# Kernel tuning notes

Hardware: AMD Instinct MI355X
Metric: run time of the kernel (lower is better)

## Reference

```python
import jax, jax.numpy as jnp
import numpy as np

B, S, HID = 1, 4096, 2048
NH, NKV, D = 16, 4, 128           # num_heads, num_kv_heads, head_dim
QPG = NH // NKV                   # q heads per kv group
GROUP = (QPG + 2) * D             # fused per-group width: Q..Q K V
TOTAL = NKV * GROUP


def setup_inputs() -> dict:
    key = jax.random.key(0)
    k0, k1, k2 = jax.random.split(key, 3)
    x = jax.random.normal(k0, (B, S, HID), dtype=jnp.float32)
    weight_qkv = jax.random.normal(k1, (TOTAL, HID), dtype=jnp.float32) * 0.02
    weight_proj = jax.random.normal(k2, (HID, NH * D), dtype=jnp.float32) * 0.02
    return {"x": x, "weight_qkv": weight_qkv, "weight_proj": weight_proj}


def reference(x, weight_qkv, weight_proj):
    b, s, _ = x.shape
    # fused QKV projection, grouped layout: [b, s, NKV, (QPG+2)*D]
    qkv = jnp.einsum('bsh,ph->bsp', x, weight_qkv).reshape(b, s, NKV, GROUP)
    q = qkv[..., : QPG * D].reshape(b, s, NKV, QPG, D)      # [b,s,g,q,d]
    k = qkv[..., QPG * D:(QPG + 1) * D]                      # [b,s,g,d]
    v = qkv[..., (QPG + 1) * D:]                             # [b,s,g,d]

    scale = 1.0 / jnp.sqrt(jnp.float32(D))
    # GQA causal attention (ring attention at cp_size=1 == full causal attn)
    scores = jnp.einsum('bsgqd,btgd->bgqst', q, k) * scale   # [b,g,q,s,s]
    causal = jnp.tril(jnp.ones((s, s), dtype=bool))
    scores = jnp.where(causal, scores, jnp.finfo(scores.dtype).min)
    attn = jax.nn.softmax(scores, axis=-1)
    out = jnp.einsum('bgqst,btgd->bsgqd', attn, v)           # [b,s,g,q,d]
    out = out.reshape(b, s, NH * D)
    return jnp.einsum('bse,he->bsh', out, weight_proj)       # [b,s,HID]
```

## Files before the change

### kernel.cpp

```cpp
#include <hip/hip_runtime.h>
#include <hip/hip_bf16.h>
#include <stdint.h>

typedef __attribute__((ext_vector_type(8))) short short8;
typedef __attribute__((ext_vector_type(4))) float f32x4;

#define S_LEN   4096
#define HID_DIM 2048
#define NHEAD   16
#define NKV     4
#define DHEAD   128
#define QPG     4
#define GROUP   768
#define TOTAL   3072

__device__ __forceinline__ ushort f2bf(float f) {
    union { float f; uint32_t u; } c; c.f = f;
    uint32_t u = c.u;
    u += 0x7fff + ((u >> 16) & 1);
    return (ushort)(u >> 16);
}

__device__ __forceinline__ void gld_lds16(const void* g, void* l) {
    __builtin_amdgcn_global_load_lds(
        (const __attribute__((address_space(1))) void*)g,
        (__attribute__((address_space(3))) void*)l, 16, 0, 0);
}

__global__ __launch_bounds__(256)
void cvt_f32_bf16(const float* __restrict__ src, ushort* __restrict__ dst,
                  int n4, int mode)
{
    int i = blockIdx.x * blockDim.x + threadIdx.x;
    int stride = gridDim.x * blockDim.x;
    for (; i < n4; i += stride) {
        float sc = 1.0f;
        if (mode == 1) {
            int row = i >> 9;
            sc = ((row % GROUP) < QPG * DHEAD) ? 0.088388347648318447f : 1.0f;
        }
        float4 v = ((const float4*)src)[i];
        ushort4 o;
        o.x = f2bf(v.x * sc); o.y = f2bf(v.y * sc);
        o.z = f2bf(v.z * sc); o.w = f2bf(v.w * sc);
        ((ushort4*)dst)[i] = o;
    }
}

__global__ __launch_bounds__(256)
void zero_f4(float4* __restrict__ p, int n4)
{
    int i = blockIdx.x * blockDim.x + threadIdx.x;
    int stride = gridDim.x * blockDim.x;
    float4 z = {0.f, 0.f, 0.f, 0.f};
    for (; i < n4; i += stride) p[i] = z;
}

__device__ __forceinline__ void store_c(ushort* C, size_t idx, float v) { C[idx] = f2bf(v); }
__device__ __forceinline__ void store_c(float*  C, size_t idx, float v) { C[idx] = v; }

template <typename OutT, bool WRITE_VT>
__global__ __launch_bounds__(256, 2)
void gemm_bt(const ushort* __restrict__ A, const ushort* __restrict__ B,
             OutT* __restrict__ C, ushort* __restrict__ VT,
             int M, int N, int K)
{
    __shared__ alignas(16) ushort Asl[128 * 32];
    __shared__ alignas(16) ushort Bsl[128 * 32];

    const int tid  = threadIdx.x;
    const int wave = tid >> 6;
    const int lane = tid & 63;
    const int quad = lane >> 4;
    const int l15  = lane & 15;
    const int wr   = wave >> 1;
    const int wc   = wave & 1;
    const int m0   = blockIdx.y * 128;
    const int n0   = blockIdx.x * 128;

    f32x4 acc[4][4];
#pragma unroll
    for (int i = 0; i < 4; i++)
#pragma unroll
        for (int j = 0; j < 4; j++) acc[i][j] = (f32x4)0.0f;

    for (int kb = 0; kb < K; kb += 32) {
        __syncthreads();
#pragma unroll
        for (int r = 0; r < 2; r++) {
            int idx = tid + r * 256;
            int row = idx >> 2, c8 = idx & 3;
            char* la = (char*)Asl + (size_t)(wave * 64 + r * 256) * 16;
            char* lb = (char*)Bsl + (size_t)(wave * 64 + r * 256) * 16;
            gld_lds16(A + (size_t)(m0 + row) * K + kb + c8 * 8, la);
            gld_lds16(B + (size_t)(n0 + row) * K + kb + c8 * 8, lb);
        }
        __syncthreads();

        short8 af[4], bf[4];
#pragma unroll
        for (int i = 0; i < 4; i++)
            af[i] = *(const short8*)(&Asl[(wr * 64 + i * 16 + l15) * 32 + quad * 8]);
#pragma unroll
        for (int j = 0; j < 4; j++)
            bf[j] = *(const short8*)(&Bsl[(wc * 64 + j * 16 + l15) * 32 + quad * 8]);
#pragma unroll
        for (int i = 0; i < 4; i++)
#pragma unroll
            for (int j = 0; j < 4; j++)
                acc[i][j] = __builtin_amdgcn_mfma_f32_16x16x32_bf16(
                    af[i], bf[j], acc[i][j], 0, 0, 0);
    }

    const bool v_block = WRITE_VT && ((n0 >> 7) % 6 == 5);
    if (!v_block) {
#pragma unroll
        for (int i = 0; i < 4; i++)
#pragma unroll
            for (int j = 0; j < 4; j++)
#pragma unroll
                for (int r = 0; r < 4; r++) {
                    int row = m0 + wr * 64 + i * 16 + quad * 4 + r;
                    int col = n0 + wc * 64 + j * 16 + l15;
                    store_c(C, (size_t)row * N + col, acc[i][j][r]);
                }
    } else {
        int g = (n0 >> 7) / 6;
#pragma unroll
        for (int i = 0; i < 4; i++)
#pragma unroll
            for (int j = 0; j < 4; j++) {
                int d    = wc * 64 + j * 16 + l15;
                int row0 = m0 + wr * 64 + i * 16 + quad * 4;
                ushort4 pk;
                pk.x = f2bf(acc[i][j][0]); pk.y = f2bf(acc[i][j][1]);
                pk.z = f2bf(acc[i][j][2]); pk.w = f2bf(acc[i][j][3]);
                *(ushort4*)(VT + (size_t)(g * 128 + d) * S_LEN + row0) = pk;
            }
    }
}

__global__ __launch_bounds__(256, 2)
void flash_attn(const ushort* __restrict__ qkv, const ushort* __restrict__ VT,
                ushort* __restrict__ out, float* __restrict__ o_slot,
                float* __restrict__ l_slot)
{
    const int b    = blockIdx.x;
    const int head = b >> 5;
    const int pair = (b >> 1) & 15;
    const int half = b & 1;
    const int g    = head >> 2;
    const int qh   = head & 3;
    const int p_h  = 31 - pair;
    const int H    = 2 * p_h + 2;
    const int slot = head * 16 + pair;

    const int tid  = threadIdx.x;
    const int wave = tid >> 6;
    const int lane = tid & 63;
    const int quad = lane >> 4;
    const int l15  = lane & 15;

    __shared__ alignas(16) ushort Kl[64][136];
    __shared__ alignas(16) ushort Vt[128][72];
    __shared__ alignas(16) ushort Pl[4][32][66];

    int seg_p[2], seg_t0[2], seg_t1[2], seg_part[2];
    int nseg;
    if (half == 0) {
        nseg = 1;
        seg_p[0] = p_h;  seg_t0[0] = 0;  seg_t1[0] = 33;           seg_part[0] = 1;
    } else {
        nseg = 2;
        seg_p[0] = p_h;  seg_t0[0] = 33; seg_t1[0] = H;            seg_part[0] = 1;
        seg_p[1] = pair; seg_t0[1] = 0;  seg_t1[1] = 2 * pair + 2; seg_part[1] = 0;
    }

    const int koff = g * GROUP + QPG * DHEAD;

    for (int s = 0; s < nseg; s++) {
        const int p  = seg_p[s];
        const int t0 = seg_t0[s];
        const int t1 = seg_t1[s];
        const int q0 = p * 128;
        const int base = q0 + wave * 32;

        short8 qf[2][4];
#pragma unroll
        for (int nq = 0; nq < 2; nq++) {
            int row = base + nq * 16 + l15;
            const ushort* qp = qkv + (size_t)row * TOTAL + g * GROUP + qh * DHEAD + quad * 8;
#pragma unroll
            for (int ks = 0; ks < 4; ks++)
                qf[nq][ks] = *(const short8*)(qp + ks * 32);
        }

        f32x4 o[2][8];
#pragma unroll
        for (int oq = 0; oq < 2; oq++)
#pragma unroll
            for (int df = 0; df < 8; df++) o[oq][df] = (f32x4)0.0f;
        float l_vec[2] = {0.0f, 0.0f};

        float4 kpre[4], vpre[4];
#pragma unroll
        for (int r = 0; r < 4; r++) {
            int c = tid + r * 256;
            int kr = c >> 4, kc = c & 15;
            kpre[r] = *(const float4*)(qkv + (size_t)(t0 * 64 + kr) * TOTAL + koff + kc * 8);
            int vd = c >> 3, vc = c & 7;
            vpre[r] = *(const float4*)(VT + (size_t)(g * 128 + vd) * S_LEN + t0 * 64 + vc * 8);
        }

        for (int t = t0; t < t1; t++) {
            __syncthreads();
#pragma unroll
            for (int r = 0; r < 4; r++) {
                int c = tid + r * 256;
                int kr = c >> 4, kc = c & 15;
                *(float4*)(&Kl[kr][kc * 8]) = kpre[r];
                int vd = c >> 3, vc = c & 7;
                *(float4*)(&Vt[vd][vc * 8]) = vpre[r];
            }
            __syncthreads();

            if (t + 1 < t1) {
                const int j1 = (t + 1) * 64;
#pragma unroll
                for (int r = 0; r < 4; r++) {
                    int c = tid + r * 256;
                    int kr = c >> 4, kc = c & 15;
                    kpre[r] = *(const float4*)(qkv + (size_t)(j1 + kr) * TOTAL + koff + kc * 8);
                    int vd = c >> 3, vc = c & 7;
                    vpre[r] = *(const float4*)(VT + (size_t)(g * 128 + vd) * S_LEN + j1 + vc * 8);
                }
            }

            const int j0 = t * 64;
            f32x4 sacc[4][2];
#pragma unroll
            for (int mk = 0; mk < 4; mk++)
#pragma unroll
                for (int nq = 0; nq < 2; nq++) sacc[mk][nq] = (f32x4)0.0f;
#pragma unroll
            for (int mk = 0; mk < 4; mk++)
#pragma unroll
                for (int ks = 0; ks < 4; ks++) {
                    short8 kf = *(const short8*)(&Kl[mk * 16 + l15][ks * 32 + quad * 8]);
#pragma unroll
                    for (int nq = 0; nq < 2; nq++)
                        sacc[mk][nq] = __builtin_amdgcn_mfma_f32_16x16x32_bf16(
                            kf, qf[nq][ks], sacc[mk][nq], 0, 0, 0);
                }

#pragma unroll
            for (int nq = 0; nq < 2; nq++) {
                const int qg = base + nq * 16 + l15;
#pragma unroll
                for (int mk = 0; mk < 4; mk++) {
                    float e0, e1, e2, e3;
                    if (j0 + mk * 16 + 15 > base + nq * 16) {
                        int kv = j0 + mk * 16 + quad * 4;
                        e0 = (kv + 0 > qg) ? 0.0f : __expf(sacc[mk][nq][0]);
                        e1 = (kv + 1 > qg) ? 0.0f : __expf(sacc[mk][nq][1]);
                        e2 = (kv + 2 > qg) ? 0.0f : __expf(sacc[mk][nq][2]);
                        e3 = (kv + 3 > qg) ? 0.0f : __expf(sacc[mk][nq][3]);
                    } else {
                        e0 = __expf(sacc[mk][nq][0]);
                        e1 = __expf(sacc[mk][nq][1]);
                        e2 = __expf(sacc[mk][nq][2]);
                        e3 = __expf(sacc[mk][nq][3]);
                    }
                    l_vec[nq] += (e0 + e1) + (e2 + e3);
                    ushort4 pk;
                    pk.x = f2bf(e0); pk.y = f2bf(e1);
                    pk.z = f2bf(e2); pk.w = f2bf(e3);
                    *(ushort4*)(&Pl[wave][nq * 16 + l15][mk * 16 + quad * 4]) = pk;
                }
            }

#pragma unroll
            for (int ks = 0; ks < 2; ks++) {
                short8 pf[2];
#pragma unroll
                for (int oq = 0; oq < 2; oq++)
                    pf[oq] = *(const short8*)(&Pl[wave][oq * 16 + l15][ks * 32 + quad * 8]);
#pragma unroll
                for (int df = 0; df < 8; df++) {
                    short8 vf = *(const short8*)(&Vt[df * 16 + l15][ks * 32 + quad * 8]);
#pragma unroll
                    for (int oq = 0; oq < 2; oq++)
                        o[oq][df] = __builtin_amdgcn_mfma_f32_16x16x32_bf16(
                            pf[oq], vf, o[oq][df], 0, 0, 0);
                }
            }
        }

        float l_full[2];
#pragma unroll
        for (int nq = 0; nq < 2; nq++) {
            float l = l_vec[nq];
            l += __shfl_xor(l, 16);
            l += __shfl_xor(l, 32);
            l_full[nq] = l;
        }

        if (seg_part[s]) {
#pragma unroll
            for (int nq = 0; nq < 2; nq++)
                if (quad == 0)
                    atomicAdd(&l_slot[slot * 128 + wave * 32 + nq * 16 + l15], l_full[nq]);
#pragma unroll
            for (int oq = 0; oq < 2; oq++)
#pragma unroll
                for (int r = 0; r < 4; r++) {
                    int row_l = wave * 32 + oq * 16 + quad * 4 + r;
#pragma unroll
                    for (int df = 0; df < 8; df++)
                        atomicAdd(&o_slot[((size_t)slot * 128 + row_l) * 128
                                          + df * 16 + l15], o[oq][df][r]);
                }
        } else {
#pragma unroll
            for (int oq = 0; oq < 2; oq++)
#pragma unroll
                for (int r = 0; r < 4; r++) {
                    float lq = __shfl(l_full[oq], quad * 4 + r);
                    float inv = 1.0f / lq;
                    int row = base + oq * 16 + quad * 4 + r;
#pragma unroll
                    for (int df = 0; df < 8; df++) {
                        float v = o[oq][df][r] * inv;
                        out[(size_t)row * (NHEAD * DHEAD) + head * DHEAD
                            + df * 16 + l15] = f2bf(v);
                    }
                }
        }
    }
}

__global__ __launch_bounds__(256)
void fixup_norm(const float* __restrict__ o_slot, const float* __restrict__ l_slot,
                ushort* __restrict__ attn)
{
    const int slot = blockIdx.x;
    const int head = slot >> 4;
    const int pair = slot & 15;
    const int q0   = (31 - pair) * 128;
    const int t    = threadIdx.x;
#pragma unroll 4
    for (int i = 0; i < 64; i++) {
        int idx = i * 256 + t;
        int row = idx >> 7, d = idx & 127;
        float l = l_slot[slot * 128 + row];
        float v = o_slot[(size_t)slot * 16384 + idx] / l;
        attn[(size_t)(q0 + row) * HID_DIM + head * DHEAD + d] = f2bf(v);
    }
}

extern "C" void kernel_launch(void* const* d_in, const int* in_sizes, int n_in,
                              void* d_out, int out_size, void* d_ws, size_t ws_size,
                              hipStream_t stream)
{
    const float* x     = (const float*)d_in[0];
    const float* wqkv  = (const float*)d_in[1];
    const float* wproj = (const float*)d_in[2];
    float* outp = (float*)d_out;

    const size_t n_x     = (size_t)S_LEN * HID_DIM;
    const size_t n_wqkv  = (size_t)TOTAL * HID_DIM;
    const size_t n_wproj = (size_t)HID_DIM * HID_DIM;
    const size_t n_qkv   = (size_t)S_LEN * TOTAL;
    const size_t n_attn  = (size_t)S_LEN * HID_DIM;

    ushort* xb     = (ushort*)d_ws;
    ushort* wqkvb  = xb + n_x;
    ushort* qkv    = wqkvb + n_wqkv;
    ushort* attn   = qkv + n_qkv;
    ushort* vt     = attn + n_attn;
    float* o_slot  = (float*)xb;
    float* l_slot  = (float*)wqkvb;
    ushort* wprojb = wqkvb;

    cvt_f32_bf16<<<2048, 256, 0, stream>>>(x, xb, (int)(n_x / 4), 0);
    cvt_f32_bf16<<<2048, 256, 0, stream>>>(wqkv, wqkvb, (int)(n_wqkv / 4), 1);

    gemm_bt<ushort, true><<<dim3(TOTAL / 128, S_LEN / 128), 256, 0, stream>>>(
        xb, wqkvb, qkv, vt, S_LEN, TOTAL, HID_DIM);

    zero_f4<<<1024, 256, 0, stream>>>((float4*)o_slot, 256 * 16384 / 4);
    zero_f4<<<64, 256, 0, stream>>>((float4*)l_slot, 256 * 128 / 4);

    flash_attn<<<512, 256, 0, stream>>>(qkv, vt, attn, o_slot, l_slot);
    fixup_norm<<<256, 256, 0, stream>>>(o_slot, l_slot, attn);

    cvt_f32_bf16<<<2048, 256, 0, stream>>>(wproj, wprojb, (int)(n_wproj / 4), 0);
    gemm_bt<float, false><<<dim3(HID_DIM / 128, S_LEN / 128), 256, 0, stream>>>(
        attn, wprojb, outp, nullptr, S_LEN, HID_DIM, HID_DIM);
}
```

Baseline: 430.5 us.

## Use exp2 softmax, per-half partial outputs, and 192-wide QKV GEMM tiles

Result: no change. 425.3 us (-1.2%).

```diff
diff --git a/kernel.cpp b/kernel.cpp
--- a/kernel.cpp
+++ b/kernel.cpp
@@ -14,11 +14,17 @@
 #define GROUP   768
 #define TOTAL   3072
 
+#define EXP2F(x) __builtin_amdgcn_exp2f(x)
+
 __device__ __forceinline__ ushort f2bf(float f) {
     union { float f; uint32_t u; } c; c.f = f;
     uint32_t u = c.u;
     u += 0x7fff + ((u >> 16) & 1);
     return (ushort)(u >> 16);
+}
+__device__ __forceinline__ float bf2f(ushort u) {
+    union { uint32_t u; float f; } c; c.u = ((uint32_t)u) << 16;
+    return c.f;
 }
 
 __device__ __forceinline__ void gld_lds16(const void* g, void* l) {
@@ -37,7 +43,7 @@
         float sc = 1.0f;
         if (mode == 1) {
             int row = i >> 9;
-            sc = ((row % GROUP) < QPG * DHEAD) ? 0.088388347648318447f : 1.0f;
+            sc = ((row % GROUP) < QPG * DHEAD) ? 0.12751744157413583f : 1.0f;
         }
         float4 v = ((const float4*)src)[i];
         ushort4 o;
@@ -47,26 +53,17 @@
     }
 }
 
-__global__ __launch_bounds__(256)
-void zero_f4(float4* __restrict__ p, int n4)
-{
-    int i = blockIdx.x * blockDim.x + threadIdx.x;
-    int stride = gridDim.x * blockDim.x;
-    float4 z = {0.f, 0.f, 0.f, 0.f};
-    for (; i < n4; i += stride) p[i] = z;
-}
-
 __device__ __forceinline__ void store_c(ushort* C, size_t idx, float v) { C[idx] = f2bf(v); }
 __device__ __forceinline__ void store_c(float*  C, size_t idx, float v) { C[idx] = v; }
 
-template <typename OutT, bool WRITE_VT>
+template <typename OutT, int NJ, bool WRITE_VT>
 __global__ __launch_bounds__(256, 2)
 void gemm_bt(const ushort* __restrict__ A, const ushort* __restrict__ B,
              OutT* __restrict__ C, ushort* __restrict__ VT,
              int M, int N, int K)
 {
     __shared__ alignas(16) ushort Asl[128 * 32];
-    __shared__ alignas(16) ushort Bsl[128 * 32];
+    __shared__ alignas(16) ushort Bsl[NJ * 32 * 32];
 
     const int tid  = threadIdx.x;
     const int wave = tid >> 6;
@@ -76,74 +73,76 @@
     const int wr   = wave >> 1;
     const int wc   = wave & 1;
     const int m0   = blockIdx.y * 128;
-    const int n0   = blockIdx.x * 128;
-
-    f32x4 acc[4][4];
+    const int n0   = blockIdx.x * (32 * NJ);
+
+    f32x4 acc[4][NJ];
 #pragma unroll
     for (int i = 0; i < 4; i++)
 #pragma unroll
-        for (int j = 0; j < 4; j++) acc[i][j] = (f32x4)0.0f;
+        for (int j = 0; j < NJ; j++) acc[i][j] = (f32x4)0.0f;
 
     for (int kb = 0; kb < K; kb += 32) {
         __syncthreads();
 #pragma unroll
-        for (int r = 0; r < 2; r++) {
-            int idx = tid + r * 256;
-            int row = idx >> 2, c8 = idx & 3;
-            char* la = (char*)Asl + (size_t)(wave * 64 + r * 256) * 16;
-            char* lb = (char*)Bsl + (size_t)(wave * 64 + r * 256) * 16;
-            gld_lds16(A + (size_t)(m0 + row) * K + kb + c8 * 8, la);
-            gld_lds16(B + (size_t)(n0 + row) * K + kb + c8 * 8, lb);
+        for (int k = 0; k < 2 + NJ / 2; k++) {
+            int idx = k * 256 + tid;
+            if (idx < 512) {
+                const ushort* g = A + (size_t)(m0 + (idx >> 2)) * K + kb + (idx & 3) * 8;
+                gld_lds16(g, (char*)Asl + (size_t)(k * 256 + wave * 64) * 16);
+            } else {
+                int j = idx - 512;
+                const ushort* g = B + (size_t)(n0 + (j >> 2)) * K + kb + (j & 3) * 8;
+                gld_lds16(g, (char*)Bsl + (size_t)((k - 2) * 256 + wave * 64) * 16);
+            }
         }
         __syncthreads();
 
-        short8 af[4], bf[4];
+        short8 af[4], bf[NJ];
 #pragma unroll
         for (int i = 0; i < 4; i++)
             af[i] = *(const short8*)(&Asl[(wr * 64 + i * 16 + l15) * 32 + quad * 8]);
 #pragma unroll
-        for (int j = 0; j < 4; j++)
-            bf[j] = *(const short8*)(&Bsl[(wc * 64 + j * 16 + l15) * 32 + quad * 8]);
+        for (int j = 0; j < NJ; j++)
+            bf[j] = *(const short8*)(&Bsl[(wc * 16 * NJ + j * 16 + l15) * 32 + quad * 8]);
 #pragma unroll
         for (int i = 0; i < 4; i++)
 #pragma unroll
-            for (int j = 0; j < 4; j++)
+            for (int j = 0; j < NJ; j++)
                 acc[i][j] = __builtin_amdgcn_mfma_f32_16x16x32_bf16(
                     af[i], bf[j], acc[i][j], 0, 0, 0);
     }
 
-    const bool v_block = WRITE_VT && ((n0 >> 7) % 6 == 5);
-    if (!v_block) {
-#pragma unroll
-        for (int i = 0; i < 4; i++)
-#pragma unroll
-            for (int j = 0; j < 4; j++)
-#pragma unroll
-                for (int r = 0; r < 4; r++) {
-                    int row = m0 + wr * 64 + i * 16 + quad * 4 + r;
-                    int col = n0 + wc * 64 + j * 16 + l15;
-                    store_c(C, (size_t)row * N + col, acc[i][j][r]);
-                }
-    } else {
-        int g = (n0 >> 7) / 6;
-#pragma unroll
-        for (int i = 0; i < 4; i++)
-#pragma unroll
-            for (int j = 0; j < 4; j++) {
-                int d    = wc * 64 + j * 16 + l15;
+#pragma unroll
+    for (int j = 0; j < NJ; j++) {
+        const int colb = n0 + wc * 16 * NJ + j * 16;
+        const int cgrp = colb % GROUP;
+        if (WRITE_VT && cgrp >= (QPG + 1) * DHEAD) {
+            const int g = colb / GROUP;
+            const int d = cgrp - (QPG + 1) * DHEAD + l15;
+#pragma unroll
+            for (int i = 0; i < 4; i++) {
                 int row0 = m0 + wr * 64 + i * 16 + quad * 4;
                 ushort4 pk;
                 pk.x = f2bf(acc[i][j][0]); pk.y = f2bf(acc[i][j][1]);
                 pk.z = f2bf(acc[i][j][2]); pk.w = f2bf(acc[i][j][3]);
                 *(ushort4*)(VT + (size_t)(g * 128 + d) * S_LEN + row0) = pk;
             }
+        } else {
+#pragma unroll
+            for (int i = 0; i < 4; i++)
+#pragma unroll
+                for (int r = 0; r < 4; r++) {
+                    int row = m0 + wr * 64 + i * 16 + quad * 4 + r;
+                    store_c(C, (size_t)row * N + colb + l15, acc[i][j][r]);
+                }
+        }
     }
 }
 
 __global__ __launch_bounds__(256, 2)
 void flash_attn(const ushort* __restrict__ qkv, const ushort* __restrict__ VT,
-                ushort* __restrict__ out, float* __restrict__ o_slot,
-                float* __restrict__ l_slot)
+                ushort* __restrict__ out, ushort* __restrict__ o_part,
+                float* __restrict__ l_part)
 {
     const int b    = blockIdx.x;
     const int head = b >> 5;
@@ -153,7 +152,7 @@
     const int qh   = head & 3;
     const int p_h  = 31 - pair;
     const int H    = 2 * p_h + 2;
-    const int slot = head * 16 + pair;
+    const int hslot = (head * 16 + pair) * 2 + half;
 
     const int tid  = threadIdx.x;
     const int wave = tid >> 6;
@@ -261,15 +260,15 @@
                     float e0, e1, e2, e3;
                     if (j0 + mk * 16 + 15 > base + nq * 16) {
                         int kv = j0 + mk * 16 + quad * 4;
-                        e0 = (kv + 0 > qg) ? 0.0f : __expf(sacc[mk][nq][0]);
-                        e1 = (kv + 1 > qg) ? 0.0f : __expf(sacc[mk][nq][1]);
-                        e2 = (kv + 2 > qg) ? 0.0f : __expf(sacc[mk][nq][2]);
-                        e3 = (kv + 3 > qg) ? 0.0f : __expf(sacc[mk][nq][3]);
+                        e0 = (kv + 0 > qg) ? 0.0f : EXP2F(sacc[mk][nq][0]);
+                        e1 = (kv + 1 > qg) ? 0.0f : EXP2F(sacc[mk][nq][1]);
+                        e2 = (kv + 2 > qg) ? 0.0f : EXP2F(sacc[mk][nq][2]);
+                        e3 = (kv + 3 > qg) ? 0.0f : EXP2F(sacc[mk][nq][3]);
                     } else {
-                        e0 = __expf(sacc[mk][nq][0]);
-                        e1 = __expf(sacc[mk][nq][1]);
-                        e2 = __expf(sacc[mk][nq][2]);
-                        e3 = __expf(sacc[mk][nq][3]);
+                        e0 = EXP2F(sacc[mk][nq][0]);
+                        e1 = EXP2F(sacc[mk][nq][1]);
+                        e2 = EXP2F(sacc[mk][nq][2]);
+                        e3 = EXP2F(sacc[mk][nq][3]);
                     }
                     l_vec[nq] += (e0 + e1) + (e2 + e3);
                     ushort4 pk;
@@ -306,10 +305,11 @@
         }
 
         if (seg_part[s]) {
+            ushort* po = o_part + (size_t)hslot * 16384;
 #pragma unroll
             for (int nq = 0; nq < 2; nq++)
                 if (quad == 0)
-                    atomicAdd(&l_slot[slot * 128 + wave * 32 + nq * 16 + l15], l_full[nq]);
+                    l_part[hslot * 128 + wave * 32 + nq * 16 + l15] = l_full[nq];
 #pragma unroll
             for (int oq = 0; oq < 2; oq++)
 #pragma unroll
@@ -317,8 +317,7 @@
                     int row_l = wave * 32 + oq * 16 + quad * 4 + r;
 #pragma unroll
                     for (int df = 0; df < 8; df++)
-                        atomicAdd(&o_slot[((size_t)slot * 128 + row_l) * 128
-                                          + df * 16 + l15], o[oq][df][r]);
+                        po[row_l * 128 + df * 16 + l15] = f2bf(o[oq][df][r]);
                 }
         } else {
 #pragma unroll
@@ -340,7 +339,7 @@
 }
 
 __global__ __launch_bounds__(256)
-void fixup_norm(const float* __restrict__ o_slot, const float* __restrict__ l_slot,
+void fixup_norm(const ushort* __restrict__ o_part, const float* __restrict__ l_part,
                 ushort* __restrict__ attn)
 {
     const int slot = blockIdx.x;
@@ -348,12 +347,14 @@
     const int pair = slot & 15;
     const int q0   = (31 - pair) * 128;
     const int t    = threadIdx.x;
+    const ushort* p0 = o_part + (size_t)(slot * 2) * 16384;
+    const ushort* p1 = p0 + 16384;
 #pragma unroll 4
     for (int i = 0; i < 64; i++) {
         int idx = i * 256 + t;
         int row = idx >> 7, d = idx & 127;
-        float l = l_slot[slot * 128 + row];
-        float v = o_slot[(size_t)slot * 16384 + idx] / l;
+        float l = l_part[(slot * 2) * 128 + row] + l_part[(slot * 2 + 1) * 128 + row];
+        float v = (bf2f(p0[idx]) + bf2f(p1[idx])) / l;
         attn[(size_t)(q0 + row) * HID_DIM + head * DHEAD + d] = f2bf(v);
     }
 }
@@ -378,23 +379,20 @@
     ushort* qkv    = wqkvb + n_wqkv;
     ushort* attn   = qkv + n_qkv;
     ushort* vt     = attn + n_attn;
-    float* o_slot  = (float*)xb;
-    float* l_slot  = (float*)wqkvb;
+    ushort* o_part = xb;
+    float*  l_part = (float*)wqkvb;
     ushort* wprojb = wqkvb;
 
     cvt_f32_bf16<<<2048, 256, 0, stream>>>(x, xb, (int)(n_x / 4), 0);
     cvt_f32_bf16<<<2048, 256, 0, stream>>>(wqkv, wqkvb, (int)(n_wqkv / 4), 1);
 
-    gemm_bt<ushort, true><<<dim3(TOTAL / 128, S_LEN / 128), 256, 0, stream>>>(
+    gemm_bt<ushort, 6, true><<<dim3(TOTAL / 192, S_LEN / 128), 256, 0, stream>>>(
         xb, wqkvb, qkv, vt, S_LEN, TOTAL, HID_DIM);
 
-    zero_f4<<<1024, 256, 0, stream>>>((float4*)o_slot, 256 * 16384 / 4);
-    zero_f4<<<64, 256, 0, stream>>>((float4*)l_slot, 256 * 128 / 4);
-
-    flash_attn<<<512, 256, 0, stream>>>(qkv, vt, attn, o_slot, l_slot);
-    fixup_norm<<<256, 256, 0, stream>>>(o_slot, l_slot, attn);
+    flash_attn<<<512, 256, 0, stream>>>(qkv, vt, attn, o_part, l_part);
+    fixup_norm<<<256, 256, 0, stream>>>(o_part, l_part, attn);
 
     cvt_f32_bf16<<<2048, 256, 0, stream>>>(wproj, wprojb, (int)(n_wproj / 4), 0);
-    gemm_bt<float, false><<<dim3(HID_DIM / 128, S_LEN / 128), 256, 0, stream>>>(
+    gemm_bt<float, 4, false><<<dim3(HID_DIM / 128, S_LEN / 128), 256, 0, stream>>>(
         attn, wprojb, outp, nullptr, S_LEN, HID_DIM, HID_DIM);
 }
```
